# Kernel tuning notes

Measured on AMD Instinct MI355X. Metric: run time of the kernel, lower is better.

The kernel has to match this reference:

```python
import math
import jax, jax.numpy as jnp
import numpy as np

CAPACITY_FACTOR = 1.0
MIN_CAPACITY = 8


def setup_inputs() -> dict:
    key = jax.random.key(0)
    k1, k2 = jax.random.split(key)
    s, d, e = 8192, 1024, 64
    inputs = jax.random.normal(k1, (s, d), dtype=jnp.float32)
    wg_weight = jax.random.normal(k2, (e, d), dtype=jnp.float32) * (1.0 / math.sqrt(d))
    return {"inputs": inputs, "wg_weight": wg_weight}


def reference(inputs, wg_weight):
    # gate projection (always fp32 in the original)
    logits = inputs.astype(jnp.float32) @ wg_weight.T  # [s, e]
    s, e = logits.shape
    # static capacity: ceil(s/e * capacity_factor), floored at min_capacity
    capacity = max(int(math.ceil(s / e * CAPACITY_FACTOR)), MIN_CAPACITY)

    gates = jax.nn.softmax(logits, axis=1)            # [s, e]
    indices = jnp.argmax(gates, axis=1)               # [s]
    mask = jax.nn.one_hot(indices, e, dtype=jnp.int32)  # [s, e]
    exp_counts = jnp.sum(mask, axis=0)                # [e]

    # load-balancing aux loss (uses mask BEFORE capacity dropping)
    me = jnp.mean(gates, axis=0)
    ce = jnp.mean(mask.astype(jnp.float32), axis=0)
    l_aux = jnp.sum(me * ce) * e

    # capacity dropping: with use_rts=False, topk over the binary mask keeps
    # the first `capacity` tokens routed to each expert, i.e. cumulative
    # position-in-expert < capacity
    positions = jnp.cumsum(mask, axis=0) - 1          # [s, e]
    mask = mask * (positions < capacity).astype(jnp.int32)

    locations = jnp.cumsum(mask, axis=0) - 1          # [s, e]
    locations_s = jnp.sum(locations * mask, axis=1)   # [s] slot per token

    gates = gates * mask.astype(jnp.float32)          # zero out dropped tokens
    locations_sc = jax.nn.one_hot(locations_s, capacity, dtype=jnp.float32)  # [s, c]
    combine_weights = jnp.einsum('se,sc->sec', gates, locations_sc)  # [s, e, c]
    dispatch_mask = combine_weights.astype(bool)
    return l_aux, combine_weights, dispatch_mask, exp_counts
```

## Files before the change

kernel.cpp:

```cpp
#include <hip/hip_runtime.h>
#include <cstdint>
#include <cstddef>

#define S 8192
#define Dm 1024
#define E 64
#define CAP 128
#define SEC 67108864ull

#define GEMM_BLOCKS 256
#define FILL_BLOCKS 2048

__global__ __launch_bounds__(256) void k_main(const float* __restrict__ x,
                                              const float* __restrict__ w,
                                              float* __restrict__ gate,
                                              int* __restrict__ idx,
                                              float* __restrict__ me_part,
                                              float* __restrict__ out) {
    int bid = blockIdx.x;
    int tid = threadIdx.x;
    if (bid < GEMM_BLOCKS) {
        __shared__ float Al[32][66];
        __shared__ float Wl[64][68];
        __shared__ float sm[32];
        __shared__ float sinv[32];
        int tok = tid & 31;
        int eo = tid >> 5;
        int t0 = bid * 32;
        const float* asrc = x + (size_t)(t0 + (tid >> 3)) * Dm + (tid & 7) * 8;
        const float* wsrc0 = w + (size_t)(tid >> 3) * Dm + (tid & 7) * 8;
        const float* wsrc1 = wsrc0 + 32 * (size_t)Dm;
        float* adst = &Al[tid >> 3][(tid & 7) * 8];
        float* wdst0 = &Wl[tid >> 3][(tid & 7) * 8];
        float* wdst1 = &Wl[32 + (tid >> 3)][(tid & 7) * 8];

        float acc[8] = {0.f, 0.f, 0.f, 0.f, 0.f, 0.f, 0.f, 0.f};
        float4 pa0 = *(const float4*)(asrc + 0);
        float4 pa1 = *(const float4*)(asrc + 4);
        float4 pw0 = *(const float4*)(wsrc0 + 0);
        float4 pw1 = *(const float4*)(wsrc0 + 4);
        float4 pw2 = *(const float4*)(wsrc1 + 0);
        float4 pw3 = *(const float4*)(wsrc1 + 4);

        for (int ch = 0; ch < 16; ++ch) {
            __syncthreads();
            *(float2*)(adst + 0) = make_float2(pa0.x, pa0.y);
            *(float2*)(adst + 2) = make_float2(pa0.z, pa0.w);
            *(float2*)(adst + 4) = make_float2(pa1.x, pa1.y);
            *(float2*)(adst + 6) = make_float2(pa1.z, pa1.w);
            *(float4*)(wdst0 + 0) = pw0;
            *(float4*)(wdst0 + 4) = pw1;
            *(float4*)(wdst1 + 0) = pw2;
            *(float4*)(wdst1 + 4) = pw3;
            __syncthreads();
            if (ch < 15) {
                int kb = (ch + 1) * 64;
                pa0 = *(const float4*)(asrc + kb);
                pa1 = *(const float4*)(asrc + kb + 4);
                pw0 = *(const float4*)(wsrc0 + kb);
                pw1 = *(const float4*)(wsrc0 + kb + 4);
                pw2 = *(const float4*)(wsrc1 + kb);
                pw3 = *(const float4*)(wsrc1 + kb + 4);
            }
#pragma unroll 4
            for (int k4 = 0; k4 < 16; ++k4) {
                float2 aa = *(const float2*)&Al[tok][k4 * 4];
                float2 ab = *(const float2*)&Al[tok][k4 * 4 + 2];
#pragma unroll
                for (int j = 0; j < 8; ++j) {
                    float4 wv = *(const float4*)&Wl[eo * 8 + j][k4 * 4];
                    acc[j] = fmaf(ab.y, wv.w, fmaf(ab.x, wv.z,
                             fmaf(aa.y, wv.y, fmaf(aa.x, wv.x, acc[j]))));
                }
            }
        }
        __syncthreads();
#pragma unroll
        for (int j = 0; j < 8; ++j) Al[tok][eo * 8 + j] = acc[j];
        __syncthreads();
        if (tid < 32) {
            float m = Al[tid][0];
            int am = 0;
#pragma unroll
            for (int c = 1; c < E; ++c) {
                float v = Al[tid][c];
                if (v > m) { m = v; am = c; }
            }
            float ssum = 0.f;
#pragma unroll
            for (int c = 0; c < E; ++c) ssum += __expf(Al[tid][c] - m);
            float inv = 1.0f / ssum;
            gate[t0 + tid] = inv;
            idx[t0 + tid] = am;
            sm[tid] = m;
            sinv[tid] = inv;
        }
        __syncthreads();
        if (tid < E) {
            float cs = 0.f;
#pragma unroll 8
            for (int r = 0; r < 32; ++r)
                cs += __expf(Al[r][tid] - sm[r]) * sinv[r];
            me_part[bid * E + tid] = cs;
        }
    } else {
        int fb = bid - GEMM_BLOCKS;
        const unsigned N4 = (unsigned)((1ull + 2ull * SEC + 64ull) / 4ull);
        float4 z = make_float4(0.f, 0.f, 0.f, 0.f);
        float4* o4 = (float4*)out;
        for (unsigned i = (unsigned)fb * 256u + tid; i < N4; i += FILL_BLOCKS * 256u)
            o4[i] = z;
    }
}

__global__ __launch_bounds__(256) void k_scan(const int* __restrict__ idx,
                                              const float* __restrict__ gate,
                                              const float* __restrict__ me_part,
                                              float* __restrict__ out) {
    int e = blockIdx.x;
    int tid = threadIdx.x;
    int lane = tid & 63;
    int wid = tid >> 6;
    __shared__ int wsum[4];
    __shared__ float red[256];
    int running = 0;
    for (int ch = 0; ch < S / 256; ++ch) {
        int t = ch * 256 + tid;
        bool f = (idx[t] == e);
        unsigned long long b = __ballot(f);
        int pre = __popcll(b & ((1ull << lane) - 1ull));
        if (lane == 0) wsum[wid] = __popcll(b);
        __syncthreads();
        int off = running;
#pragma unroll
        for (int w2 = 0; w2 < 4; ++w2)
            if (w2 < wid) off += wsum[w2];
        int p = off + pre;
        if (f && p < CAP) {
            size_t o = 1 + (size_t)t * (E * CAP) + (size_t)e * CAP + (size_t)p;
            out[o] = gate[t];
            out[o + (size_t)SEC] = 1.0f;
        }
        running += wsum[0] + wsum[1] + wsum[2] + wsum[3];
        __syncthreads();
    }
    red[tid] = me_part[tid * E + e];
    __syncthreads();
    for (int s2 = 128; s2 > 0; s2 >>= 1) {
        if (tid < s2) red[tid] += red[tid + s2];
        __syncthreads();
    }
    if (tid == 0) {
        out[1 + 2 * (size_t)SEC + e] = (float)running;
        float la = red[0] * (1.0f / (float)S) *
                   ((float)running / (float)S) * (float)E;
        atomicAdd(out, la);
    }
}

extern "C" void kernel_launch(void* const* d_in, const int* in_sizes, int n_in,
                              void* d_out, int out_size, void* d_ws, size_t ws_size,
                              hipStream_t stream) {
    const float* x = (const float*)d_in[0];
    const float* w = (const float*)d_in[1];
    float* out = (float*)d_out;

    float* me_part = (float*)d_ws;
    float* gate = me_part + GEMM_BLOCKS * E;
    int* idx = (int*)(gate + S);

    k_main<<<dim3(GEMM_BLOCKS + FILL_BLOCKS), dim3(256), 0, stream>>>(
        x, w, gate, idx, me_part, out);
    k_scan<<<dim3(64), dim3(256), 0, stream>>>(idx, gate, me_part, out);
}
```

Measured before the change: 140.8 us.

## Double gate-GEMM token tile per block and use nontemporal stores for zero fill

Each GEMM block now handles 64 tokens instead of 32, so there are half as many GEMM blocks and each thread keeps 16 accumulators, which doubles reuse of the staged weight tile. The zero fill of the large output switches to nontemporal vector stores to avoid polluting the cache. The scan kernel's reduction is guarded for the smaller number of partial sums. Larger per-thread register use may lower occupancy, and fewer GEMM blocks give less parallelism on the critical path.

```diff
diff --git a/kernel.cpp b/kernel.cpp
--- a/kernel.cpp
+++ b/kernel.cpp
@@ -8,8 +8,10 @@
 #define CAP 128
 #define SEC 67108864ull
 
-#define GEMM_BLOCKS 256
+#define GEMM_BLOCKS 128
 #define FILL_BLOCKS 2048
+
+typedef float f32x4 __attribute__((ext_vector_type(4)));
 
 __global__ __launch_bounds__(256) void k_main(const float* __restrict__ x,
                                               const float* __restrict__ w,
@@ -20,23 +22,31 @@
     int bid = blockIdx.x;
     int tid = threadIdx.x;
     if (bid < GEMM_BLOCKS) {
-        __shared__ float Al[32][66];
+        __shared__ float Al[64][66];
         __shared__ float Wl[64][68];
-        __shared__ float sm[32];
-        __shared__ float sinv[32];
-        int tok = tid & 31;
-        int eo = tid >> 5;
-        int t0 = bid * 32;
-        const float* asrc = x + (size_t)(t0 + (tid >> 3)) * Dm + (tid & 7) * 8;
-        const float* wsrc0 = w + (size_t)(tid >> 3) * Dm + (tid & 7) * 8;
+        __shared__ float sm[64];
+        __shared__ float sinv[64];
+        int tok = tid & 63;
+        int eo = tid >> 6;
+        int t0 = bid * 64;
+        int r = tid >> 3;
+        int c = (tid & 7) * 8;
+        const float* asrc0 = x + (size_t)(t0 + r) * Dm + c;
+        const float* asrc1 = asrc0 + 32 * (size_t)Dm;
+        const float* wsrc0 = w + (size_t)r * Dm + c;
         const float* wsrc1 = wsrc0 + 32 * (size_t)Dm;
-        float* adst = &Al[tid >> 3][(tid & 7) * 8];
-        float* wdst0 = &Wl[tid >> 3][(tid & 7) * 8];
-        float* wdst1 = &Wl[32 + (tid >> 3)][(tid & 7) * 8];
+        float* adst0 = &Al[r][c];
+        float* adst1 = &Al[32 + r][c];
+        float* wdst0 = &Wl[r][c];
+        float* wdst1 = &Wl[32 + r][c];
 
-        float acc[8] = {0.f, 0.f, 0.f, 0.f, 0.f, 0.f, 0.f, 0.f};
-        float4 pa0 = *(const float4*)(asrc + 0);
-        float4 pa1 = *(const float4*)(asrc + 4);
+        float acc[16];
+#pragma unroll
+        for (int i = 0; i < 16; ++i) acc[i] = 0.f;
+        float4 pa0 = *(const float4*)(asrc0 + 0);
+        float4 pa1 = *(const float4*)(asrc0 + 4);
+        float4 pa2 = *(const float4*)(asrc1 + 0);
+        float4 pa3 = *(const float4*)(asrc1 + 4);
         float4 pw0 = *(const float4*)(wsrc0 + 0);
         float4 pw1 = *(const float4*)(wsrc0 + 4);
         float4 pw2 = *(const float4*)(wsrc1 + 0);
@@ -44,10 +54,14 @@
 
         for (int ch = 0; ch < 16; ++ch) {
             __syncthreads();
-            *(float2*)(adst + 0) = make_float2(pa0.x, pa0.y);
-            *(float2*)(adst + 2) = make_float2(pa0.z, pa0.w);
-            *(float2*)(adst + 4) = make_float2(pa1.x, pa1.y);
-            *(float2*)(adst + 6) = make_float2(pa1.z, pa1.w);
+            *(float2*)(adst0 + 0) = make_float2(pa0.x, pa0.y);
+            *(float2*)(adst0 + 2) = make_float2(pa0.z, pa0.w);
+            *(float2*)(adst0 + 4) = make_float2(pa1.x, pa1.y);
+            *(float2*)(adst0 + 6) = make_float2(pa1.z, pa1.w);
+            *(float2*)(adst1 + 0) = make_float2(pa2.x, pa2.y);
+            *(float2*)(adst1 + 2) = make_float2(pa2.z, pa2.w);
+            *(float2*)(adst1 + 4) = make_float2(pa3.x, pa3.y);
+            *(float2*)(adst1 + 6) = make_float2(pa3.z, pa3.w);
             *(float4*)(wdst0 + 0) = pw0;
             *(float4*)(wdst0 + 4) = pw1;
             *(float4*)(wdst1 + 0) = pw2;
@@ -55,20 +69,22 @@
             __syncthreads();
             if (ch < 15) {
                 int kb = (ch + 1) * 64;
-                pa0 = *(const float4*)(asrc + kb);
-                pa1 = *(const float4*)(asrc + kb + 4);
+                pa0 = *(const float4*)(asrc0 + kb);
+                pa1 = *(const float4*)(asrc0 + kb + 4);
+                pa2 = *(const float4*)(asrc1 + kb);
+                pa3 = *(const float4*)(asrc1 + kb + 4);
                 pw0 = *(const float4*)(wsrc0 + kb);
                 pw1 = *(const float4*)(wsrc0 + kb + 4);
                 pw2 = *(const float4*)(wsrc1 + kb);
                 pw3 = *(const float4*)(wsrc1 + kb + 4);
             }
-#pragma unroll 4
+#pragma unroll 2
             for (int k4 = 0; k4 < 16; ++k4) {
                 float2 aa = *(const float2*)&Al[tok][k4 * 4];
                 float2 ab = *(const float2*)&Al[tok][k4 * 4 + 2];
 #pragma unroll
-                for (int j = 0; j < 8; ++j) {
-                    float4 wv = *(const float4*)&Wl[eo * 8 + j][k4 * 4];
+                for (int j = 0; j < 16; ++j) {
+                    float4 wv = *(const float4*)&Wl[eo * 16 + j][k4 * 4];
                     acc[j] = fmaf(ab.y, wv.w, fmaf(ab.x, wv.z,
                              fmaf(aa.y, wv.y, fmaf(aa.x, wv.x, acc[j]))));
                 }
@@ -76,19 +92,19 @@
         }
         __syncthreads();
 #pragma unroll
-        for (int j = 0; j < 8; ++j) Al[tok][eo * 8 + j] = acc[j];
+        for (int j = 0; j < 16; ++j) Al[tok][eo * 16 + j] = acc[j];
         __syncthreads();
-        if (tid < 32) {
+        if (tid < 64) {
             float m = Al[tid][0];
             int am = 0;
 #pragma unroll
-            for (int c = 1; c < E; ++c) {
-                float v = Al[tid][c];
-                if (v > m) { m = v; am = c; }
+            for (int cc = 1; cc < E; ++cc) {
+                float v = Al[tid][cc];
+                if (v > m) { m = v; am = cc; }
             }
             float ssum = 0.f;
 #pragma unroll
-            for (int c = 0; c < E; ++c) ssum += __expf(Al[tid][c] - m);
+            for (int cc = 0; cc < E; ++cc) ssum += __expf(Al[tid][cc] - m);
             float inv = 1.0f / ssum;
             gate[t0 + tid] = inv;
             idx[t0 + tid] = am;
@@ -99,17 +115,17 @@
         if (tid < E) {
             float cs = 0.f;
 #pragma unroll 8
-            for (int r = 0; r < 32; ++r)
-                cs += __expf(Al[r][tid] - sm[r]) * sinv[r];
+            for (int rr = 0; rr < 64; ++rr)
+                cs += __expf(Al[rr][tid] - sm[rr]) * sinv[rr];
             me_part[bid * E + tid] = cs;
         }
     } else {
         int fb = bid - GEMM_BLOCKS;
         const unsigned N4 = (unsigned)((1ull + 2ull * SEC + 64ull) / 4ull);
-        float4 z = make_float4(0.f, 0.f, 0.f, 0.f);
-        float4* o4 = (float4*)out;
+        f32x4 z = {0.f, 0.f, 0.f, 0.f};
+        f32x4* o4 = (f32x4*)out;
         for (unsigned i = (unsigned)fb * 256u + tid; i < N4; i += FILL_BLOCKS * 256u)
-            o4[i] = z;
+            __builtin_nontemporal_store(z, o4 + i);
     }
 }
 
@@ -144,7 +160,7 @@
         running += wsum[0] + wsum[1] + wsum[2] + wsum[3];
         __syncthreads();
     }
-    red[tid] = me_part[tid * E + e];
+    red[tid] = (tid < GEMM_BLOCKS) ? me_part[tid * E + e] : 0.f;
     __syncthreads();
     for (int s2 = 128; s2 > 0; s2 >>= 1) {
         if (tid < s2) red[tid] += red[tid + s2];
```

New measurement: 159.5 us. 13.3% more time.
